# Kernel tuning notes

Measured on AMD Instinct MI355X. Metric: run time of the kernel, lower is better.

Reference implementation:

```python
import jax, jax.numpy as jnp
import numpy as np

N_HEAD = 4
GROUPS = 4
EPS = 1e-5


def group_norm(x, w, b):
    # x: [B, C, D, H, W], normalized over (C//GROUPS, D, H, W) per group
    B, C = x.shape[0], x.shape[1]
    xr = x.reshape(B, GROUPS, -1)
    mu = xr.mean(axis=2, keepdims=True)
    var = xr.var(axis=2, keepdims=True)
    xn = ((xr - mu) * jax.lax.rsqrt(var + EPS)).reshape(x.shape)
    return xn * w.reshape(1, C, 1, 1, 1) + b.reshape(1, C, 1, 1, 1)


def conv3d(x, w, b, pad):
    y = jax.lax.conv_general_dilated(
        x, w, window_strides=(1, 1, 1), padding=[(pad, pad)] * 3,
        dimension_numbers=('NCDHW', 'OIDHW', 'NCDHW'))
    return y + b.reshape(1, -1, 1, 1, 1)


def upsample_nearest(x, size):
    # torch nearest: out index i maps to floor(i * in / out)
    out = x
    for ax in (2, 3, 4):
        n_in = out.shape[ax]
        idx = (jnp.arange(size) * n_in) // size
        out = jnp.take(out, idx, axis=ax)
    return out


def setup_inputs() -> dict:
    key = jax.random.key(0)
    ks = jax.random.split(key, 8)
    B, C, D, H, W = 2, 256, 32, 32, 32
    inp = {
        'q': jax.random.normal(ks[0], (B, C, D, H, W), jnp.float32),
        'k': jax.random.normal(ks[1], (B, C, D, H, W), jnp.float32),
        'v': jax.random.normal(ks[2], (B, C, D, H, W), jnp.float32),
        'gn_w': jnp.ones((C,), jnp.float32),
        'gn_b': jnp.zeros((C,), jnp.float32),
        'out_w': jax.random.normal(ks[3], (C, C, 1, 1, 1), jnp.float32) * 0.02,
        'out_b': jnp.zeros((C,), jnp.float32),
        'dg_w': jax.random.normal(ks[4], (3, C, 3, 3, 3), jnp.float32) * 0.02,
        'dg_b': jnp.zeros((3,), jnp.float32),
        'nl_w': jax.random.normal(ks[5], (3, 3, 3, 3, 3), jnp.float32) * 0.02,
        'nl_b': jnp.zeros((3,), jnp.float32),
        'size': 64,
    }
    return inp


def reference(q, k, v, gn_w, gn_b, out_w, out_b, dg_w, dg_b, nl_w, nl_b, size):
    B, C, D, H, W = q.shape
    c = C // N_HEAD
    n = D * H * W
    residual = q
    nq = group_norm(q, gn_w, gn_b)
    nk = group_norm(k, gn_w, gn_b)
    nv = group_norm(v, gn_w, gn_b)
    qh = nq.reshape(B, N_HEAD, c, n)
    kh = jax.nn.softmax(nk.reshape(B, N_HEAD, c, n), axis=-1)
    vh = nv.reshape(B, N_HEAD, c, n)
    # linear attention: context over spatial tokens, then project q
    context = jnp.einsum('bhdn,bhen->bhde', kh, vh)      # [B,H,c,c]
    out = jnp.einsum('bhde,bhdn->bhen', context, qh)     # [B,H,c,n]
    out = out.reshape(B, C, D, H, W)
    out = conv3d(out, out_w, out_b, pad=0)
    out = conv3d(out + residual, dg_w, dg_b, pad=1)      # [B,3,D,H,W]
    out = upsample_nearest(out, size)                    # [B,3,size,size,size]
    out = conv3d(out, nl_w, nl_b, pad=1)
    return out
```

## Files before the change

### kernel.cpp

```cpp
#include <hip/hip_runtime.h>
#include <math.h>

typedef unsigned int uint32;
typedef unsigned short u16;

typedef __bf16 bf16x8 __attribute__((ext_vector_type(8)));
typedef float f32x4 __attribute__((ext_vector_type(4)));

#define OFF_STATS 0
#define OFF_MUSR  64
#define OFF_L     128
#define OFF_MROW  640
#define OFF_MAXV  1280
#define OFF_MINV  1792
#define OFF_CTX   2048
#define OFF_MBT   34816
#define OFF_KB    165888
#define OFF_Z     167936
#define OFF_DG    8556544
#define OFF_CTXP  8753152
#define OFF_LP    10850304
#define OFF_DGP   8753152
#define WS_PART_FLOATS 15044608

__device__ __forceinline__ float bf2f(u16 h){ return __uint_as_float(((uint32)h)<<16); }
__device__ __forceinline__ u16 f2bf(float f){ uint32 u=__float_as_uint(f); return (u16)((u + 0x7fffu + ((u>>16)&1u))>>16); }

__global__ __launch_bounds__(512) void k_stats(const float* __restrict__ q, const float* __restrict__ k,
                                               const float* __restrict__ v, float* __restrict__ ws){
  int gid = blockIdx.x >> 6;
  int chunk = blockIdx.x & 63;
  int t = gid >> 3; int bg = gid & 7;
  const float* src = (t==0)? q : ((t==1)? k : v);
  const float* base = src + (size_t)bg*2097152 + (size_t)chunk*32768;
  int tid = threadIdx.x;
  float s=0.f, ss=0.f, mx=-INFINITY, mn=INFINITY;
  #pragma unroll
  for (int it=0; it<8; ++it){
    float4 x = *(const float4*)(base + it*4096 + tid*8);
    float4 y = *(const float4*)(base + it*4096 + tid*8 + 4);
    s += ((x.x+x.y)+(x.z+x.w)) + ((y.x+y.y)+(y.z+y.w));
    ss = fmaf(x.x,x.x, fmaf(x.y,x.y, fmaf(x.z,x.z, fmaf(x.w,x.w, ss))));
    ss = fmaf(y.x,y.x, fmaf(y.y,y.y, fmaf(y.z,y.z, fmaf(y.w,y.w, ss))));
    mx = fmaxf(mx, fmaxf(fmaxf(fmaxf(x.x,x.y), fmaxf(x.z,x.w)), fmaxf(fmaxf(y.x,y.y), fmaxf(y.z,y.w))));
    mn = fminf(mn, fminf(fminf(fminf(x.x,x.y), fminf(x.z,x.w)), fminf(fminf(y.x,y.y), fminf(y.z,y.w))));
  }
  for (int o=32;o>0;o>>=1){
    s  += __shfl_down(s,o);  ss += __shfl_down(ss,o);
    mx = fmaxf(mx, __shfl_down(mx,o)); mn = fminf(mn, __shfl_down(mn,o));
  }
  __shared__ float rsum[8], rssq[8], rmx[8], rmn[8];
  int w = tid>>6;
  if ((tid&63)==0){ rsum[w]=s; rssq[w]=ss; rmx[w]=mx; rmn[w]=mn; }
  __syncthreads();
  if (tid==0){
    float fs = ((rsum[0]+rsum[1])+(rsum[2]+rsum[3])) + ((rsum[4]+rsum[5])+(rsum[6]+rsum[7]));
    float fq = ((rssq[0]+rssq[1])+(rssq[2]+rssq[3])) + ((rssq[4]+rssq[5])+(rssq[6]+rssq[7]));
    atomicAdd(&ws[OFF_STATS + gid*2],   fs);
    atomicAdd(&ws[OFF_STATS + gid*2+1], fq);
    if (t==1){
      int r = bg*64 + chunk;
      float fmx = fmaxf(fmaxf(fmaxf(rmx[0],rmx[1]),fmaxf(rmx[2],rmx[3])),
                        fmaxf(fmaxf(rmx[4],rmx[5]),fmaxf(rmx[6],rmx[7])));
      float fmn = fminf(fminf(fminf(rmn[0],rmn[1]),fminf(rmn[2],rmn[3])),
                        fminf(fminf(rmn[4],rmn[5]),fminf(rmn[6],rmn[7])));
      ws[OFF_MAXV + r] = fmx;
      ws[OFF_MINV + r] = fmn;
    }
  }
}

__global__ void k_finalize(const float* __restrict__ gw, const float* __restrict__ gb, float* __restrict__ ws){
  int tid = threadIdx.x;
  if (tid < 24){
    float s=ws[OFF_STATS+2*tid], ss=ws[OFF_STATS+2*tid+1];
    const float inv = 1.f/2097152.f;
    float mu = s*inv;
    float var = ss*inv - mu*mu;
    ws[OFF_MUSR+2*tid]=mu; ws[OFF_MUSR+2*tid+1]=rsqrtf(var+1e-5f);
  }
  __syncthreads();
  if (tid < 512){
    int b=tid>>8, c=tid&255, g=c>>6;
    int gi = 8 + b*4 + g;
    float mu=ws[OFF_MUSR+2*gi], rs=ws[OFF_MUSR+2*gi+1];
    float a = rs*gw[c]; float beta = gb[c] - mu*a;
    float mx = ws[OFF_MAXV+tid], mn = ws[OFF_MINV+tid];
    ws[OFF_MROW+tid] = (a>=0.f)? fmaf(a,mx,beta) : fmaf(a,mn,beta);
  }
}

__device__ __forceinline__ float4 expaff(float4 x, float a, float b, float& s){
  float4 e;
  e.x=__expf(fmaf(x.x,a,b)); e.y=__expf(fmaf(x.y,a,b));
  e.z=__expf(fmaf(x.z,a,b)); e.w=__expf(fmaf(x.w,a,b));
  s += (e.x+e.y)+(e.z+e.w);
  return e;
}
__device__ __forceinline__ float4 aff4(float4 x, float a, float b){
  return make_float4(fmaf(x.x,a,b), fmaf(x.y,a,b), fmaf(x.z,a,b), fmaf(x.w,a,b));
}
__device__ __forceinline__ bf16x8 cvt8(float4 a, float4 b){
  bf16x8 r;
  r[0]=(__bf16)a.x; r[1]=(__bf16)a.y; r[2]=(__bf16)a.z; r[3]=(__bf16)a.w;
  r[4]=(__bf16)b.x; r[5]=(__bf16)b.y; r[6]=(__bf16)b.z; r[7]=(__bf16)b.w;
  return r;
}

__global__ __launch_bounds__(256) void k_ctx(const float* __restrict__ kk, const float* __restrict__ vv,
                                             const float* __restrict__ gw, const float* __restrict__ gb,
                                             float* __restrict__ ws, int usePart){
  int chunk = blockIdx.x;
  int bh = blockIdx.y; int b=bh>>2, h=bh&3;
  int tid = threadIdx.x;
  int lane = tid & 63, wv = tid >> 6;
  int m16 = lane & 15, quad = lane >> 4;
  int dhalf = wv >> 1, ehalf = wv & 1;

  int gik = 8+bh, giv = 16+bh;
  float muk=ws[OFF_MUSR+2*gik], rsk=ws[OFF_MUSR+2*gik+1];
  float muv=ws[OFF_MUSR+2*giv], rsv=ws[OFF_MUSR+2*giv+1];
  float akr[2], bmkr[2], avr[2], bvvr[2];
  #pragma unroll
  for (int t=0;t<2;++t){
    int c = h*64 + dhalf*32 + t*16 + m16;
    float a = rsk*gw[c];
    akr[t]=a; bmkr[t]=(gb[c]-muk*a) - ws[OFF_MROW + b*256 + c];
  }
  #pragma unroll
  for (int t=0;t<2;++t){
    int c = h*64 + ehalf*32 + t*16 + m16;
    float a = rsv*gw[c];
    avr[t]=a; bvvr[t]=gb[c]-muv*a;
  }

  const float* kb = kk + (size_t)b*8388608 + (size_t)h*2097152;
  const float* vb = vv + (size_t)b*8388608 + (size_t)h*2097152;
  int nb0 = chunk*512;
  const float* kp[2]; const float* vp[2];
  kp[0] = kb + (size_t)(dhalf*32 + m16)*32768 + nb0 + quad*8;
  kp[1] = kp[0] + (size_t)16*32768;
  vp[0] = vb + (size_t)(ehalf*32 + m16)*32768 + nb0 + quad*8;
  vp[1] = vp[0] + (size_t)16*32768;

  f32x4 acc[2][2];
  #pragma unroll
  for (int i=0;i<2;++i){
    #pragma unroll
    for (int j=0;j<2;++j) acc[i][j] = 0.f;
  }
  float lsum[2] = {0.f, 0.f};

#define KCTX_LOAD(DK, DV, OFFS) do { \
    _Pragma("unroll") \
    for (int t=0;t<2;++t){ \
      DK[t][0] = *(const float4*)(kp[t] + (OFFS)); \
      DK[t][1] = *(const float4*)(kp[t] + (OFFS) + 4); \
      DV[t][0] = *(const float4*)(vp[t] + (OFFS)); \
      DV[t][1] = *(const float4*)(vp[t] + (OFFS) + 4); \
    } } while(0)

#define KCTX_STEP(SK, SV) do { \
    bf16x8 afr[2], bfr[2]; \
    _Pragma("unroll") \
    for (int t=0;t<2;++t){ \
      float4 e0 = expaff(SK[t][0], akr[t], bmkr[t], lsum[t]); \
      float4 e1 = expaff(SK[t][1], akr[t], bmkr[t], lsum[t]); \
      afr[t] = cvt8(e0,e1); \
      float4 v0 = aff4(SV[t][0], avr[t], bvvr[t]); \
      float4 v1 = aff4(SV[t][1], avr[t], bvvr[t]); \
      bfr[t] = cvt8(v0,v1); \
    } \
    _Pragma("unroll") \
    for (int i=0;i<2;++i){ \
      _Pragma("unroll") \
      for (int j=0;j<2;++j) \
        acc[i][j] = __builtin_amdgcn_mfma_f32_16x16x32_bf16(afr[i], bfr[j], acc[i][j], 0, 0, 0); \
    } } while(0)

  float4 ka[2][2], va[2][2];
  KCTX_LOAD(ka, va, 0);
  for (int s=0; s<15; ++s){
    float4 kn[2][2], vn[2][2];
    KCTX_LOAD(kn, vn, (s+1)*32);
    KCTX_STEP(ka, va);
    #pragma unroll
    for (int t=0;t<2;++t){
      ka[t][0]=kn[t][0]; ka[t][1]=kn[t][1];
      va[t][0]=vn[t][0]; va[t][1]=vn[t][1];
    }
  }
  KCTX_STEP(ka, va);
#undef KCTX_LOAD
#undef KCTX_STEP

  #pragma unroll
  for (int t=0;t<2;++t){
    lsum[t] += __shfl_down(lsum[t], 16);
    lsum[t] += __shfl_down(lsum[t], 32);
  }

  if (usePart){
    float* cp = ws + OFF_CTXP + (size_t)(chunk*8+bh)*4096;
    #pragma unroll
    for (int i=0;i<2;++i){
      #pragma unroll
      for (int j=0;j<2;++j){
        int row0 = dhalf*32 + i*16 + quad*4;
        int col  = ehalf*32 + j*16 + m16;
        #pragma unroll
        for (int r=0;r<4;++r)
          cp[(row0+r)*64 + col] = acc[i][j][r];
      }
    }
    if (ehalf==0 && quad==0){
      #pragma unroll
      for (int t=0;t<2;++t)
        ws[OFF_LP + (chunk*8+bh)*64 + dhalf*32 + t*16 + m16] = lsum[t];
    }
  } else {
    float* cp = ws + OFF_CTX + (size_t)bh*4096;
    #pragma unroll
    for (int i=0;i<2;++i){
      #pragma unroll
      for (int j=0;j<2;++j){
        int row0 = dhalf*32 + i*16 + quad*4;
        int col  = ehalf*32 + j*16 + m16;
        #pragma unroll
        for (int r=0;r<4;++r)
          atomicAdd(&cp[(row0+r)*64 + col], acc[i][j][r]);
      }
    }
    if (ehalf==0 && quad==0){
      #pragma unroll
      for (int t=0;t<2;++t)
        atomicAdd(&ws[OFF_L + bh*64 + dhalf*32 + t*16 + m16], lsum[t]);
    }
  }
}

__global__ void k_ctxred(float* __restrict__ ws){
  int i = blockIdx.x*256 + threadIdx.x;
  if (i < 32768){
    float s = 0.f;
    const float* p = ws + OFF_CTXP + i;
    #pragma unroll 8
    for (int c=0;c<64;++c) s += p[(size_t)c*32768];
    ws[OFF_CTX + i] = s;
  } else if (i < 33280){
    int j = i - 32768;
    float s=0.f; const float* p = ws + OFF_LP + j;
    #pragma unroll 8
    for (int c=0;c<64;++c) s += p[c*512];
    ws[OFF_L + j] = s;
  }
}

__global__ __launch_bounds__(256) void k_weff(const float* __restrict__ w1, const float* __restrict__ ob,
                                              const float* __restrict__ gw, const float* __restrict__ gb,
                                              float* __restrict__ ws){
  int co = blockIdx.x; int b = blockIdx.y;
  int cp = threadIdx.x;
  int hp = cp>>6, dp = cp&63;
  const float* ctx = ws + OFF_CTX + (size_t)(b*4+hp)*4096 + dp*64;
  const float* w1p = w1 + co*256 + hp*64;
  float s = 0.f;
  #pragma unroll 8
  for (int e=0;e<64;++e) s = fmaf(w1p[e], ctx[e], s);
  float L = ws[OFF_L + b*256 + cp];
  float weff = s / L;
  int gi = b*4 + hp;
  float mu = ws[OFF_MUSR+2*gi], rs = ws[OFF_MUSR+2*gi+1];
  float aq = rs*gw[cp]; float bq = gb[cp] - mu*aq;
  u16* mbp = (u16*)(ws + OFF_MBT);
  mbp[(size_t)b*65536 + (size_t)co*256 + cp] = f2bf(weff*aq);
  float kp = weff*bq;
  for (int o=32;o>0;o>>=1) kp += __shfl_down(kp,o);
  __shared__ float red[4];
  if ((cp&63)==0) red[cp>>6]=kp;
  __syncthreads();
  if (cp==0) ws[OFF_KB + b*256 + co] = ob[co] + ((red[0]+red[1])+(red[2]+red[3]));
}

__global__ __launch_bounds__(256, 4) void k_z(const float* __restrict__ q, float* __restrict__ ws){
  extern __shared__ char smem[];
  u16* As = (u16*)smem;
  u16* Bs = As + 128*72;
  u16* Cs = (u16*)smem;
  int nt = blockIdx.x, cot = blockIdx.y, b = blockIdx.z;
  int n0 = nt*128, co0 = cot*128;
  int tid = threadIdx.x;
  int lane = tid & 63, wv = tid >> 6;
  int m16 = lane & 15, quad = lane >> 4;
  int wco = (wv>>1)*64, wn = (wv&1)*64;
  const u16* mb = (const u16*)(ws + OFF_MBT) + (size_t)b*65536;
  const float* qb = q + (size_t)b*8388608;
  f32x4 acc[4][4];
  #pragma unroll
  for (int i=0;i<4;++i){
    #pragma unroll
    for (int j=0;j<4;++j) acc[i][j] = 0.f;
  }
  int r2 = tid>>1, seg = tid&1;
  int nq = tid & 31, cp0 = tid >> 5;
  for (int kt=0; kt<4; ++kt){
    {
      const u16* src = mb + (size_t)(co0 + r2)*256 + kt*64 + seg*32;
      u16* dst = As + r2*72 + seg*32;
      uint4 w0 = *(const uint4*)(src);
      uint4 w1 = *(const uint4*)(src+8);
      uint4 w2 = *(const uint4*)(src+16);
      uint4 w3 = *(const uint4*)(src+24);
      *(uint4*)(dst)    = w0; *(uint4*)(dst+8)  = w1;
      *(uint4*)(dst+16) = w2; *(uint4*)(dst+24) = w3;
    }
    #pragma unroll
    for (int p=0;p<4;++p){
      int cpair = cp0 + 8*p;
      int c = kt*64 + 2*cpair;
      const float* q0 = qb + (size_t)c*32768 + n0 + nq;
      const float* q1 = q0 + 32768;
      #pragma unroll
      for (int i=0;i<4;++i){
        float a  = q0[32*i];
        float bb = q1[32*i];
        uint32 dw = (uint32)f2bf(a) | ((uint32)f2bf(bb)<<16);
        *(uint32*)(Bs + (nq+32*i)*72 + 2*cpair) = dw;
      }
    }
    __syncthreads();
    #pragma unroll
    for (int ks=0; ks<2; ++ks){
      bf16x8 af[4], bfr[4];
      #pragma unroll
      for (int i=0;i<4;++i) af[i]  = *(const bf16x8*)(As + (wco + i*16 + m16)*72 + ks*32 + quad*8);
      #pragma unroll
      for (int j=0;j<4;++j) bfr[j] = *(const bf16x8*)(Bs + (wn + j*16 + m16)*72 + ks*32 + quad*8);
      #pragma unroll
      for (int i=0;i<4;++i){
        #pragma unroll
        for (int j=0;j<4;++j)
          acc[i][j] = __builtin_amdgcn_mfma_f32_16x16x32_bf16(af[i], bfr[j], acc[i][j], 0, 0, 0);
      }
    }
    __syncthreads();
  }
  #pragma unroll
  for (int i=0;i<4;++i){
    #pragma unroll
    for (int r=0;r<4;++r){
      int row = wco + i*16 + quad*4 + r;
      #pragma unroll
      for (int j=0;j<4;++j)
        Cs[row*136 + wn + j*16 + m16] = f2bf(acc[i][j][r]);
    }
  }
  __syncthreads();
  {
    int co = co0 + r2;
    float kbv = ws[OFF_KB + b*256 + co];
    u16* zp = (u16*)(ws + OFF_Z) + (size_t)b*8388608 + (size_t)co*32768 + n0 + seg*64;
    const float* qr = qb + (size_t)co*32768 + n0 + seg*64;
    #pragma unroll
    for (int ch=0; ch<8; ++ch){
      uint4 cv = *(const uint4*)(Cs + r2*136 + seg*64 + ch*8);
      float4 qa = *(const float4*)(qr + ch*8);
      float4 qc = *(const float4*)(qr + ch*8 + 4);
      float z0 = qa.x + bf2f((u16)(cv.x&0xffff)) + kbv;
      float z1 = qa.y + bf2f((u16)(cv.x>>16))    + kbv;
      float z2 = qa.z + bf2f((u16)(cv.y&0xffff)) + kbv;
      float z3 = qa.w + bf2f((u16)(cv.y>>16))    + kbv;
      float z4 = qc.x + bf2f((u16)(cv.z&0xffff)) + kbv;
      float z5 = qc.y + bf2f((u16)(cv.z>>16))    + kbv;
      float z6 = qc.z + bf2f((u16)(cv.w&0xffff)) + kbv;
      float z7 = qc.w + bf2f((u16)(cv.w>>16))    + kbv;
      uint4 u;
      u.x = (uint32)f2bf(z0) | ((uint32)f2bf(z1)<<16);
      u.y = (uint32)f2bf(z2) | ((uint32)f2bf(z3)<<16);
      u.z = (uint32)f2bf(z4) | ((uint32)f2bf(z5)<<16);
      u.w = (uint32)f2bf(z6) | ((uint32)f2bf(z7)<<16);
      *(uint4*)(zp + ch*8) = u;
    }
  }
}

__global__ __launch_bounds__(256) void k_dg(const float* __restrict__ dgw, float* __restrict__ ws, int usePart){
  int tile = blockIdx.x;
  int split = blockIdx.y;
  int b = blockIdx.z;
  int d0 = (tile>>1)*8, h0=(tile&1)*16;
  int tid = threadIdx.x;
  int wt = tid&1, hy=(tid>>1)&15, dx=tid>>5;
  int d = d0+dx, h = h0+hy, w0 = wt*16;
  int cbeg = split*8;
  __shared__ float wss[8][27][4];
  for (int i=tid;i<864;i+=256){
    int ci = i/108; int r = i - ci*108; int tap = r>>2; int o = r&3;
    wss[ci][tap][o] = (o<3)? dgw[o*6912 + (cbeg+ci)*27 + tap] : 0.f;
  }
  __syncthreads();
  const u16* zp = (const u16*)(ws+OFF_Z) + (size_t)b*8388608;
  float acc[3][16];
  #pragma unroll
  for (int o=0;o<3;++o){
    #pragma unroll
    for (int j=0;j<16;++j) acc[o][j]=0.f;
  }
  for (int ci=0; ci<8; ++ci){
    const u16* zc = zp + (size_t)(cbeg+ci)*32768;
    #pragma unroll
    for (int kd=0;kd<3;++kd){
      int gd = d+kd-1;
      #pragma unroll
      for (int kh=0;kh<3;++kh){
        int gh = h+kh-1;
        bool rv = (gd>=0) & (gd<32) & (gh>=0) & (gh<32);
        const u16* rowp = zc + gd*1024 + gh*32 + w0;
        uint4 u0 = *(const uint4*)(rowp);
        uint4 u1 = *(const uint4*)(rowp+8);
        u16 le = (wt==0)? (u16)0 : rowp[-1];
        u16 ri = (wt==1)? (u16)0 : rowp[16];
        if (!rv){ u0 = make_uint4(0,0,0,0); u1 = make_uint4(0,0,0,0); le = 0; ri = 0; }
        float r[18];
        r[0]  = bf2f(le);
        r[1]  = bf2f((u16)(u0.x&0xffff)); r[2]  = bf2f((u16)(u0.x>>16));
        r[3]  = bf2f((u16)(u0.y&0xffff)); r[4]  = bf2f((u16)(u0.y>>16));
        r[5]  = bf2f((u16)(u0.z&0xffff)); r[6]  = bf2f((u16)(u0.z>>16));
        r[7]  = bf2f((u16)(u0.w&0xffff)); r[8]  = bf2f((u16)(u0.w>>16));
        r[9]  = bf2f((u16)(u1.x&0xffff)); r[10] = bf2f((u16)(u1.x>>16));
        r[11] = bf2f((u16)(u1.y&0xffff)); r[12] = bf2f((u16)(u1.y>>16));
        r[13] = bf2f((u16)(u1.z&0xffff)); r[14] = bf2f((u16)(u1.z>>16));
        r[15] = bf2f((u16)(u1.w&0xffff)); r[16] = bf2f((u16)(u1.w>>16));
        r[17] = bf2f(ri);
        #pragma unroll
        for (int kw=0;kw<3;++kw){
          float4 wv = *(const float4*)&wss[ci][kd*9+kh*3+kw][0];
          #pragma unroll
          for (int j=0;j<16;++j){
            acc[0][j]=fmaf(r[j+kw],wv.x,acc[0][j]);
            acc[1][j]=fmaf(r[j+kw],wv.y,acc[1][j]);
            acc[2][j]=fmaf(r[j+kw],wv.z,acc[2][j]);
          }
        }
      }
    }
  }
  if (usePart){
    float* op = ws + OFF_DGP + (size_t)split*196608 + (size_t)b*98304;
    #pragma unroll
    for (int o=0;o<3;++o){
      int base = o*32768 + d*1024 + h*32 + w0;
      *(float4*)&op[base+0]  = make_float4(acc[o][0],acc[o][1],acc[o][2],acc[o][3]);
      *(float4*)&op[base+4]  = make_float4(acc[o][4],acc[o][5],acc[o][6],acc[o][7]);
      *(float4*)&op[base+8]  = make_float4(acc[o][8],acc[o][9],acc[o][10],acc[o][11]);
      *(float4*)&op[base+12] = make_float4(acc[o][12],acc[o][13],acc[o][14],acc[o][15]);
    }
  } else {
    float* op = ws + OFF_DG + (size_t)b*98304;
    #pragma unroll
    for (int o=0;o<3;++o){
      #pragma unroll
      for (int j=0;j<16;++j)
        atomicAdd(&op[o*32768 + d*1024 + h*32 + w0 + j], acc[o][j]);
    }
  }
}

__global__ void k_dgred(float* __restrict__ ws){
  int i = blockIdx.x*256 + threadIdx.x;
  float s = 0.f;
  const float* p = ws + OFF_DGP + i;
  #pragma unroll 8
  for (int c=0;c<32;++c) s += p[(size_t)c*196608];
  ws[OFF_DG + i] = s;
}

__global__ __launch_bounds__(256) void k_up(const float* __restrict__ dgb, const float* __restrict__ nlw,
                                            const float* __restrict__ nlb, const float* __restrict__ ws,
                                            float* __restrict__ out){
  int b = blockIdx.y; int tileIdx = blockIdx.x;
  int zt0 = (tileIdx&7)*8, yt0 = ((tileIdx>>3)&7)*8, xt0 = (tileIdx>>6)*4;
  int sx0 = (xt0>>1)-1, sy0 = (yt0>>1)-1, sz0 = (zt0>>1)-1;
  __shared__ float ds[3][4][6][6];
  __shared__ float wl[243];
  const float* dgp = ws + OFF_DG + (size_t)b*98304;
  for (int i=threadIdx.x; i<432; i+=256){
    int ch = i/144; int r = i-ch*144; int sx=r/36; int rr=r-sx*36; int sy=rr/6; int sz=rr-sy*6;
    int gx = sx0+sx, gy = sy0+sy, gz = sz0+sz;
    float v=0.f;
    if (gx>=0&&gx<32&&gy>=0&&gy<32&&gz>=0&&gz<32) v = dgp[ch*32768 + gx*1024 + gy*32 + gz] + dgb[ch];
    ds[ch][sx][sy][sz] = v;
  }
  for (int i=threadIdx.x;i<243;i+=256) wl[i] = nlw[i];
  __syncthreads();
  int zt = threadIdx.x&7, yt=(threadIdx.x>>3)&7, xt=threadIdx.x>>6;
  int x = xt0+xt, y=yt0+yt, zc=zt0+zt;
  float a0=nlb[0], a1=nlb[1], a2=nlb[2];
  #pragma unroll
  for (int i=0;i<3;++i){
    #pragma unroll
    for (int kd=0;kd<3;++kd){
      int sxi = ((x+kd-1)>>1) - sx0;
      #pragma unroll
      for (int kh=0;kh<3;++kh){
        int syi = ((y+kh-1)>>1) - sy0;
        #pragma unroll
        for (int kw=0;kw<3;++kw){
          int szi = ((zc+kw-1)>>1) - sz0;
          float vv = ds[i][sxi][syi][szi];
          int tap = kd*9+kh*3+kw;
          a0 = fmaf(vv, wl[i*27+tap],      a0);
          a1 = fmaf(vv, wl[81+i*27+tap],   a1);
          a2 = fmaf(vv, wl[162+i*27+tap],  a2);
        }
      }
    }
  }
  size_t o0 = (size_t)b*786432 + (size_t)x*4096 + y*64 + zc;
  out[o0] = a0; out[o0+262144] = a1; out[o0+524288] = a2;
}

extern "C" void kernel_launch(void* const* d_in, const int* in_sizes, int n_in,
                              void* d_out, int out_size, void* d_ws, size_t ws_size,
                              hipStream_t stream){
  const float* q    = (const float*)d_in[0];
  const float* k    = (const float*)d_in[1];
  const float* v    = (const float*)d_in[2];
  const float* gnw  = (const float*)d_in[3];
  const float* gnb  = (const float*)d_in[4];
  const float* outw = (const float*)d_in[5];
  const float* outb = (const float*)d_in[6];
  const float* dgw  = (const float*)d_in[7];
  const float* dgb  = (const float*)d_in[8];
  const float* nlw  = (const float*)d_in[9];
  const float* nlb  = (const float*)d_in[10];
  float* out = (float*)d_out;
  float* ws  = (float*)d_ws;
  int usePart = (ws_size >= (size_t)WS_PART_FLOATS*4) ? 1 : 0;

  (void)hipMemsetAsync(ws, 0, 139264, stream);
  (void)hipMemsetAsync((void*)(ws + OFF_DG), 0, 196608*4, stream);

  k_stats   <<<dim3(1536),   dim3(512), 0, stream>>>(q,k,v,ws);
  k_finalize<<<dim3(1),      dim3(512), 0, stream>>>(gnw,gnb,ws);
  k_ctx     <<<dim3(64,8),   dim3(256), 0, stream>>>(k,v,gnw,gnb,ws,usePart);
  if (usePart) k_ctxred<<<dim3(130), dim3(256), 0, stream>>>(ws);
  k_weff    <<<dim3(256,2),  dim3(256), 0, stream>>>(outw,outb,gnw,gnb,ws);
  k_z       <<<dim3(256,2,2),dim3(256), 36864, stream>>>(q,ws);
  k_dg      <<<dim3(8,32,2), dim3(256), 0, stream>>>(dgw,ws,usePart);
  if (usePart) k_dgred<<<dim3(768), dim3(256), 0, stream>>>(ws);
  k_up      <<<dim3(1024,2), dim3(256), 0, stream>>>(dgb,nlw,nlb,ws,out);
}
```

Before: 401.3 us.

## Move q group-norm stats into k_ctx grid and drop softmax max-shift

Computes the q GroupNorm statistics inside extra blocks of the k_ctx launch instead of in k_stats, so the q read overlaps with the context computation. k_weff now derives q's mean and rstd directly from the raw sums. The per-row max/min tracking used to shift the softmax exponent is removed, so exp is applied to the unshifted normalized k. This trims one kernel's work but risks overflow for large normalized k values and relies on the input range being moderate.

```diff
diff --git a/kernel.cpp b/kernel.cpp
--- a/kernel.cpp
+++ b/kernel.cpp
@@ -26,15 +26,16 @@
 __device__ __forceinline__ float bf2f(u16 h){ return __uint_as_float(((uint32)h)<<16); }
 __device__ __forceinline__ u16 f2bf(float f){ uint32 u=__float_as_uint(f); return (u16)((u + 0x7fffu + ((u>>16)&1u))>>16); }
 
-__global__ __launch_bounds__(512) void k_stats(const float* __restrict__ q, const float* __restrict__ k,
+__global__ __launch_bounds__(512) void k_stats(const float* __restrict__ k,
                                                const float* __restrict__ v, float* __restrict__ ws){
-  int gid = blockIdx.x >> 6;
+  int gid8 = blockIdx.x >> 6;
   int chunk = blockIdx.x & 63;
-  int t = gid >> 3; int bg = gid & 7;
-  const float* src = (t==0)? q : ((t==1)? k : v);
+  int gid = 8 + gid8;
+  const float* src = (gid8 < 8)? k : v;
+  int bg = gid8 & 7;
   const float* base = src + (size_t)bg*2097152 + (size_t)chunk*32768;
   int tid = threadIdx.x;
-  float s=0.f, ss=0.f, mx=-INFINITY, mn=INFINITY;
+  float s=0.f, ss=0.f;
   #pragma unroll
   for (int it=0; it<8; ++it){
     float4 x = *(const float4*)(base + it*4096 + tid*8);
@@ -42,51 +43,30 @@
     s += ((x.x+x.y)+(x.z+x.w)) + ((y.x+y.y)+(y.z+y.w));
     ss = fmaf(x.x,x.x, fmaf(x.y,x.y, fmaf(x.z,x.z, fmaf(x.w,x.w, ss))));
     ss = fmaf(y.x,y.x, fmaf(y.y,y.y, fmaf(y.z,y.z, fmaf(y.w,y.w, ss))));
-    mx = fmaxf(mx, fmaxf(fmaxf(fmaxf(x.x,x.y), fmaxf(x.z,x.w)), fmaxf(fmaxf(y.x,y.y), fmaxf(y.z,y.w))));
-    mn = fminf(mn, fminf(fminf(fminf(x.x,x.y), fminf(x.z,x.w)), fminf(fminf(y.x,y.y), fminf(y.z,y.w))));
   }
   for (int o=32;o>0;o>>=1){
     s  += __shfl_down(s,o);  ss += __shfl_down(ss,o);
-    mx = fmaxf(mx, __shfl_down(mx,o)); mn = fminf(mn, __shfl_down(mn,o));
-  }
-  __shared__ float rsum[8], rssq[8], rmx[8], rmn[8];
+  }
+  __shared__ float rsum[8], rssq[8];
   int w = tid>>6;
-  if ((tid&63)==0){ rsum[w]=s; rssq[w]=ss; rmx[w]=mx; rmn[w]=mn; }
+  if ((tid&63)==0){ rsum[w]=s; rssq[w]=ss; }
   __syncthreads();
   if (tid==0){
     float fs = ((rsum[0]+rsum[1])+(rsum[2]+rsum[3])) + ((rsum[4]+rsum[5])+(rsum[6]+rsum[7]));
     float fq = ((rssq[0]+rssq[1])+(rssq[2]+rssq[3])) + ((rssq[4]+rssq[5])+(rssq[6]+rssq[7]));
     atomicAdd(&ws[OFF_STATS + gid*2],   fs);
     atomicAdd(&ws[OFF_STATS + gid*2+1], fq);
-    if (t==1){
-      int r = bg*64 + chunk;
-      float fmx = fmaxf(fmaxf(fmaxf(rmx[0],rmx[1]),fmaxf(rmx[2],rmx[3])),
-                        fmaxf(fmaxf(rmx[4],rmx[5]),fmaxf(rmx[6],rmx[7])));
-      float fmn = fminf(fminf(fminf(rmn[0],rmn[1]),fminf(rmn[2],rmn[3])),
-                        fminf(fminf(rmn[4],rmn[5]),fminf(rmn[6],rmn[7])));
-      ws[OFF_MAXV + r] = fmx;
-      ws[OFF_MINV + r] = fmn;
-    }
-  }
-}
-
-__global__ void k_finalize(const float* __restrict__ gw, const float* __restrict__ gb, float* __restrict__ ws){
+  }
+}
+
+__global__ void k_finalize(float* __restrict__ ws){
   int tid = threadIdx.x;
-  if (tid < 24){
+  if (tid >= 8 && tid < 24){
     float s=ws[OFF_STATS+2*tid], ss=ws[OFF_STATS+2*tid+1];
     const float inv = 1.f/2097152.f;
     float mu = s*inv;
     float var = ss*inv - mu*mu;
     ws[OFF_MUSR+2*tid]=mu; ws[OFF_MUSR+2*tid+1]=rsqrtf(var+1e-5f);
-  }
-  __syncthreads();
-  if (tid < 512){
-    int b=tid>>8, c=tid&255, g=c>>6;
-    int gi = 8 + b*4 + g;
-    float mu=ws[OFF_MUSR+2*gi], rs=ws[OFF_MUSR+2*gi+1];
-    float a = rs*gw[c]; float beta = gb[c] - mu*a;
-    float mx = ws[OFF_MAXV+tid], mn = ws[OFF_MINV+tid];
-    ws[OFF_MROW+tid] = (a>=0.f)? fmaf(a,mx,beta) : fmaf(a,mn,beta);
   }
 }
 
@@ -107,12 +87,37 @@
   return r;
 }
 
-__global__ __launch_bounds__(256) void k_ctx(const float* __restrict__ kk, const float* __restrict__ vv,
+__global__ __launch_bounds__(256) void k_ctx(const float* __restrict__ qq,
+                                             const float* __restrict__ kk, const float* __restrict__ vv,
                                              const float* __restrict__ gw, const float* __restrict__ gb,
                                              float* __restrict__ ws, int usePart){
+  int tid = threadIdx.x;
+  if (blockIdx.y >= 8){
+    int sblk = (blockIdx.y - 8)*64 + blockIdx.x;
+    int row0 = sblk*2;
+    int half = tid>>7, l = tid&127;
+    const float* p = qq + (size_t)(row0+half)*32768 + l*4;
+    float s=0.f, ss=0.f;
+    #pragma unroll 8
+    for (int it=0; it<64; ++it){
+      float4 x = *(const float4*)(p + it*512);
+      s += (x.x+x.y)+(x.z+x.w);
+      ss = fmaf(x.x,x.x, fmaf(x.y,x.y, fmaf(x.z,x.z, fmaf(x.w,x.w, ss))));
+    }
+    for (int o=32;o>0;o>>=1){ s += __shfl_down(s,o); ss += __shfl_down(ss,o); }
+    __shared__ float rs_[4], rq_[4];
+    if ((tid&63)==0){ rs_[tid>>6]=s; rq_[tid>>6]=ss; }
+    __syncthreads();
+    if (tid==0){
+      int gid = (row0>>8)*4 + ((row0>>6)&3);
+      atomicAdd(&ws[OFF_STATS + 2*gid],   (rs_[0]+rs_[1])+(rs_[2]+rs_[3]));
+      atomicAdd(&ws[OFF_STATS + 2*gid+1], (rq_[0]+rq_[1])+(rq_[2]+rq_[3]));
+    }
+    return;
+  }
+
   int chunk = blockIdx.x;
   int bh = blockIdx.y; int b=bh>>2, h=bh&3;
-  int tid = threadIdx.x;
   int lane = tid & 63, wv = tid >> 6;
   int m16 = lane & 15, quad = lane >> 4;
   int dhalf = wv >> 1, ehalf = wv & 1;
@@ -125,7 +130,7 @@
   for (int t=0;t<2;++t){
     int c = h*64 + dhalf*32 + t*16 + m16;
     float a = rsk*gw[c];
-    akr[t]=a; bmkr[t]=(gb[c]-muk*a) - ws[OFF_MROW + b*256 + c];
+    akr[t]=a; bmkr[t]=gb[c]-muk*a;
   }
   #pragma unroll
   for (int t=0;t<2;++t){
@@ -270,7 +275,11 @@
   float L = ws[OFF_L + b*256 + cp];
   float weff = s / L;
   int gi = b*4 + hp;
-  float mu = ws[OFF_MUSR+2*gi], rs = ws[OFF_MUSR+2*gi+1];
+  float sq_  = ws[OFF_STATS + 2*gi];
+  float sqq_ = ws[OFF_STATS + 2*gi + 1];
+  const float invN = 1.f/2097152.f;
+  float mu = sq_*invN;
+  float rs = rsqrtf(sqq_*invN - mu*mu + 1e-5f);
   float aq = rs*gw[cp]; float bq = gb[cp] - mu*aq;
   u16* mbp = (u16*)(ws + OFF_MBT);
   mbp[(size_t)b*65536 + (size_t)co*256 + cp] = f2bf(weff*aq);
@@ -541,9 +550,9 @@
   (void)hipMemsetAsync(ws, 0, 139264, stream);
   (void)hipMemsetAsync((void*)(ws + OFF_DG), 0, 196608*4, stream);
 
-  k_stats   <<<dim3(1536),   dim3(512), 0, stream>>>(q,k,v,ws);
-  k_finalize<<<dim3(1),      dim3(512), 0, stream>>>(gnw,gnb,ws);
-  k_ctx     <<<dim3(64,8),   dim3(256), 0, stream>>>(k,v,gnw,gnb,ws,usePart);
+  k_stats   <<<dim3(1024),   dim3(512), 0, stream>>>(k,v,ws);
+  k_finalize<<<dim3(1),      dim3(32),  0, stream>>>(ws);
+  k_ctx     <<<dim3(64,12),  dim3(256), 0, stream>>>(q,k,v,gnw,gnb,ws,usePart);
   if (usePart) k_ctxred<<<dim3(130), dim3(256), 0, stream>>>(ws);
   k_weff    <<<dim3(256,2),  dim3(256), 0, stream>>>(outw,outb,gnw,gnb,ws);
   k_z       <<<dim3(256,2,2),dim3(256), 36864, stream>>>(q,ws);
```

Result: faster. 386.1 us (median of 2 runs) (-3.8%).
